# Optimization experiments

Hardware: AMD Instinct MI355X
Metric: run time of the kernel (lower is better)

The kernel has to match this reference:

```python
import jax, jax.numpy as jnp
import numpy as np

NPOINT = 1024   # number of sampled centers
NSAMPLE = 32    # neighbors per center
BN_EPS = 1e-5


def setup_inputs() -> dict:
    key = jax.random.key(0)
    ks = jax.random.split(key, 6)
    B, N, C = 8, 4096, 6
    inp = {
        "xyz": jax.random.normal(ks[0], (B, N, 3), jnp.float32),
        "points": jax.random.normal(ks[1], (B, N, C), jnp.float32),
        "W0": jax.random.normal(ks[2], (64, 9), jnp.float32) * 0.1,
        "g0": jnp.ones((64,), jnp.float32),
        "b0": jnp.zeros((64,), jnp.float32),
        "W1": jax.random.normal(ks[3], (64, 64), jnp.float32) * 0.1,
        "g1": jnp.ones((64,), jnp.float32),
        "b1": jnp.zeros((64,), jnp.float32),
        "W2": jax.random.normal(ks[4], (128, 64), jnp.float32) * 0.1,
        "g2": jnp.ones((128,), jnp.float32),
        "b2": jnp.zeros((128,), jnp.float32),
    }
    return inp


def sample_and_group(xyz, points):
    # xyz: [B,N,3], points: [B,N,C]
    B, N, _ = xyz.shape
    stride = N // NPOINT
    new_xyz = xyz[:, ::stride]                      # [B,S,3] deterministic subsample (FPS surrogate)
    # squared pairwise distances via ||a||^2 + ||b||^2 - 2 a.b  -> [B,S,N]
    d = (jnp.sum(new_xyz * new_xyz, -1)[:, :, None]
         + jnp.sum(xyz * xyz, -1)[:, None, :]
         - 2.0 * jnp.einsum('bsd,bnd->bsn', new_xyz, xyz))
    _, idx = jax.lax.top_k(-d, NSAMPLE)             # [B,S,K] KNN indices
    gather = jax.vmap(lambda arr, i: arr[i])        # per-batch gather: [N,C],[S,K] -> [S,K,C]
    g_xyz = gather(xyz, idx) - new_xyz[:, :, None, :]   # relative coords [B,S,K,3]
    g_pts = gather(points, idx)                     # [B,S,K,C]
    new_points = jnp.concatenate([g_xyz, g_pts], -1)    # [B,S,K,3+C]
    return new_xyz, new_points


def mlp_layer(x, W, g, b):
    # Conv2d(1x1, bias=False) == channel contraction; BN2d with batch stats; ReLU
    x = jnp.einsum('bskc,oc->bsko', x, W)
    m = jnp.mean(x, axis=(0, 1, 2))
    v = jnp.var(x, axis=(0, 1, 2))
    x = (x - m) * jax.lax.rsqrt(v + BN_EPS) * g + b
    return jax.nn.relu(x)


def reference(xyz, points, W0, g0, b0, W1, g1, b1, W2, g2, b2):
    new_xyz, x = sample_and_group(xyz, points)      # x: [B,S,K,9]
    x = mlp_layer(x, W0, g0, b0)
    x = mlp_layer(x, W1, g1, b1)
    x = mlp_layer(x, W2, g2, b2)
    new_points = jnp.max(x, axis=2)                 # max-pool over neighbor dim K -> [B,S,128]
    return new_xyz, new_points
```

## Files before the change

kernel.cpp:

```cpp
#include <hip/hip_runtime.h>
#include <float.h>
#include <stdint.h>

#define TOT   262144
#define NPTS  4096
#define KNN   32
#define BN_EPS 1e-5f
#define CAPV  64
#define TILEP 2048

typedef _Float16 f16;
typedef _Float16 f16x2 __attribute__((ext_vector_type(2)));
typedef _Float16 f16x4 __attribute__((ext_vector_type(4)));
typedef _Float16 f16x8 __attribute__((ext_vector_type(8)));
typedef float    f32x4 __attribute__((ext_vector_type(4)));

__device__ __forceinline__ int mbcnt64(unsigned long long m){
  return __builtin_amdgcn_mbcnt_hi((unsigned)(m>>32),
         __builtin_amdgcn_mbcnt_lo((unsigned)(m & 0xffffffffull), 0));
}
__device__ __forceinline__ unsigned f2ord(float f){
  unsigned u = __float_as_uint(f);
  return u ^ (((unsigned)((int)u >> 31)) | 0x80000000u);
}
__device__ __forceinline__ f16x2 bnrelu2(f16x2 x, f16x2 a, f16x2 c){
  f16x2 r = x*a + c;
  const f16 z = (f16)0.f;
  r[0] = r[0] > z ? r[0] : z;
  r[1] = r[1] > z ? r[1] : z;
  return r;
}
__device__ __forceinline__ void writeElem(int n, int e, float qx, float qy, float qz,
    const float* __restrict__ xb3, const float* __restrict__ fb,
    f16* __restrict__ grouped, f16* __restrict__ g16){
  float px = xb3[n*3+0], py = xb3[n*3+1], pz = xb3[n*3+2];
  f16 a[16];
  a[0]=(f16)(px-qx); a[1]=(f16)(py-qy); a[2]=(f16)(pz-qz);
  #pragma unroll
  for (int c6=0;c6<6;c6++) a[3+c6] = (f16)fb[n*6+c6];
  #pragma unroll
  for (int i=9;i<16;i++) a[i]=(f16)0.f;
  #pragma unroll
  for (int c=0;c<9;c++) grouped[c*TOT+e] = a[c];
  f16x8 lo, hi;
  #pragma unroll
  for (int i=0;i<8;i++){ lo[i]=a[i]; hi[i]=a[8+i]; }
  *(f16x8*)(g16 + (size_t)e*16)     = lo;
  *(f16x8*)(g16 + (size_t)e*16 + 8) = hi;
}

__global__ __launch_bounds__(256) void knn_gather(
    const float* __restrict__ xyz, const float* __restrict__ pts,
    f16* __restrict__ grouped, f16* __restrict__ g16,
    float* __restrict__ out_newxyz){
  __shared__ float4 tile[TILEP];
  __shared__ unsigned wk[8][CAPV];
  __shared__ unsigned short wi[8][CAPV];
  __shared__ unsigned lcnt[8];
  const int tid = threadIdx.x, lane = tid & 63, wv = tid >> 6;
  const int q0 = blockIdx.x*8 + wv*2;
  const int b  = (blockIdx.x*8) >> 10;
  const float* xb3 = xyz + (size_t)b*NPTS*3;
  float qx[2],qy[2],qz[2],qq[2];
  #pragma unroll
  for (int t=0;t<2;t++){
    int n = ((q0+t) & 1023)*4;
    qx[t]=xb3[n*3+0]; qy[t]=xb3[n*3+1]; qz[t]=xb3[n*3+2];
    qq[t]=qx[t]*qx[t]+qy[t]*qy[t]+qz[t]*qz[t];
  }
  if (tid < 8) lcnt[tid] = 0;
  if (lane == 0){
    #pragma unroll
    for (int t=0;t<2;t++){
      out_newxyz[(q0+t)*3+0]=qx[t]; out_newxyz[(q0+t)*3+1]=qy[t];
      out_newxyz[(q0+t)*3+2]=qz[t];
    }
  }

  float dmin[2] = {FLT_MAX, FLT_MAX};
  #pragma unroll 1
  for (int r=0; r<2; ++r){
    __syncthreads();
    #pragma unroll
    for (int k=0;k<8;k++){
      int p = r*TILEP + k*256 + tid;
      float x = xb3[p*3+0], y = xb3[p*3+1], z = xb3[p*3+2];
      tile[k*256+tid] = make_float4(x,y,z, x*x+y*y+z*z);
    }
    __syncthreads();
    #pragma unroll 4
    for (int i=0;i<32;i++){
      float4 P = tile[i*64+lane];
      #pragma unroll
      for (int t=0;t<2;t++){
        float d = (qq[t]+P.w) - 2.f*(qx[t]*P.x+qy[t]*P.y+qz[t]*P.z);
        dmin[t] = d < dmin[t] ? d : dmin[t];
      }
    }
  }
  float sm[2] = {dmin[0], dmin[1]};
  #pragma unroll
  for (int k=2;k<=64;k<<=1){
    #pragma unroll
    for (int j=k>>1;j>0;j>>=1){
      bool keepmin = (((lane&k)==0) == ((lane&j)==0));
      #pragma unroll
      for (int t=0;t<2;t++){
        float o = __shfl_xor(sm[t], j, 64);
        sm[t] = keepmin ? fminf(sm[t],o) : fmaxf(sm[t],o);
      }
    }
  }
  float Uf[2];
  #pragma unroll
  for (int t=0;t<2;t++) Uf[t] = __shfl(sm[t], 31, 64);

  #pragma unroll 1
  for (int r=0; r<2; ++r){
    __syncthreads();
    #pragma unroll
    for (int k=0;k<8;k++){
      int p = r*TILEP + k*256 + tid;
      float x = xb3[p*3+0], y = xb3[p*3+1], z = xb3[p*3+2];
      tile[k*256+tid] = make_float4(x,y,z, x*x+y*y+z*z);
    }
    __syncthreads();
    #pragma unroll 2
    for (int i=0;i<32;i++){
      float4 P = tile[i*64+lane];
      #pragma unroll
      for (int t=0;t<2;t++){
        float d = (qq[t]+P.w) - 2.f*(qx[t]*P.x+qy[t]*P.y+qz[t]*P.z);
        if (d <= Uf[t]){
          unsigned p2 = atomicAdd(&lcnt[wv*2+t], 1u);
          if (p2 < CAPV){
            wk[wv*2+t][p2] = f2ord(d);
            wi[wv*2+t][p2] = (unsigned short)(r*TILEP + i*64 + lane);
          }
        }
      }
    }
  }
  int cnt[2] = {(int)lcnt[wv*2], (int)lcnt[wv*2+1]};

  unsigned long long v[2];
  #pragma unroll
  for (int t=0;t<2;t++){
    unsigned myk = (lane<cnt[t]) ? wk[wv*2+t][lane] : 0xFFFFFFFFu;
    unsigned myi = (lane<cnt[t]) ? wi[wv*2+t][lane] : 0u;
    v[t] = (((unsigned long long)myk)<<16) | myi;
  }
  #pragma unroll
  for (int k=2;k<=64;k<<=1){
    #pragma unroll
    for (int j=k>>1;j>0;j>>=1){
      bool keepmin = (((lane&k)==0) == ((lane&j)==0));
      #pragma unroll
      for (int t=0;t<2;t++){
        unsigned long long o = __shfl_xor(v[t], j, 64);
        v[t] = keepmin ? (v[t]<o?v[t]:o) : (v[t]>o?v[t]:o);
      }
    }
  }

  const float* fb = pts + (size_t)b*NPTS*6;
  #pragma unroll 1
  for (int t=0;t<2;t++){
    const int ebase = (q0+t)*KNN;
    if (cnt[t] <= CAPV){
      if (lane < KNN){
        int n = (int)(v[t] & 0xffffull);
        writeElem(n, ebase+lane, qx[t],qy[t],qz[t], xb3, fb, grouped, g16);
      }
    } else {
      unsigned V=0;
      for (int bit=31; bit>=0; --bit){
        unsigned X = V | (1u<<bit);
        int c=0;
        for (int j=0;j<64;j++){
          int n = j*64+lane;
          float px=xb3[n*3], py=xb3[n*3+1], pz=xb3[n*3+2];
          float d = qq[t] + (px*px+py*py+pz*pz)
                  - 2.f*(qx[t]*px+qy[t]*py+qz[t]*pz);
          c += __popcll(__ballot(f2ord(d) < X));
        }
        if (c < KNN) V = X;
      }
      int cnt2=0;
      for (int pass=0; pass<2; ++pass){
        for (int j=0;j<64;j++){
          int n = j*64+lane;
          float px=xb3[n*3], py=xb3[n*3+1], pz=xb3[n*3+2];
          float d = qq[t] + (px*px+py*py+pz*pz)
                  - 2.f*(qx[t]*px+qy[t]*py+qz[t]*pz);
          unsigned kk = f2ord(d);
          bool sel = pass ? (kk==V) : (kk<V);
          unsigned long long msk = __ballot(sel);
          int pos = cnt2 + mbcnt64(msk);
          if (sel && pos < KNN)
            writeElem(n, ebase+pos, qx[t],qy[t],qz[t], xb3, fb, grouped, g16);
          cnt2 += __popcll(msk);
        }
      }
    }
  }
}

__global__ __launch_bounds__(256) void stats0m(const f16* __restrict__ grouped,
    float* __restrict__ s0m){
  const int lane = threadIdx.x & 63, wv = threadIdx.x >> 6;
  const int c = lane & 15, q = lane >> 4;
  const int base = (blockIdx.x*4 + wv)*512;
  f16x8 cfill = {};
  if (c == 9){
    #pragma unroll
    for (int i=0;i<8;i++) cfill[i] = (f16)1.f;
  }
  f32x4 acc = {0.f,0.f,0.f,0.f};
  #pragma unroll 4
  for (int chunk=0; chunk<16; ++chunk){
    int e = base + chunk*32 + q*8;
    f16x8 f = cfill;
    if (c < 9) f = *(const f16x8*)(grouped + (size_t)c*TOT + e);
    acc = __builtin_amdgcn_mfma_f32_16x16x32_f16(f, f, acc, 0,0,0);
  }
  __shared__ float red[4][16][16];
  #pragma unroll
  for (int i=0;i<4;i++) red[wv][q*4+i][c] = acc[i];
  __syncthreads();
  const int tid = threadIdx.x;
  if (tid < 160){
    int row = tid>>4, col = tid&15;
    float vv = red[0][row][col]+red[1][row][col]+red[2][row][col]+red[3][row][col];
    atomicAdd(&s0m[tid], vv);
  }
}

__global__ void finalize0(const float* __restrict__ s0m,
    const float* __restrict__ W0, const float* __restrict__ g0,
    const float* __restrict__ b0, float* __restrict__ ac0,
    const float* __restrict__ W1, const float* __restrict__ W2,
    f16* __restrict__ W0h, f16* __restrict__ W1h, f16* __restrict__ W2h){
  const int tid = threadIdx.x;
  __shared__ float S[160];
  __shared__ float A0s[64];
  if (tid < 160) S[tid] = s0m[tid];
  __syncthreads();
  if (tid < 64){
    float w[9];
    #pragma unroll
    for (int c=0;c<9;c++) w[c]=W0[tid*9+c];
    const float inv = 1.f/(float)TOT;
    float m=0.f;
    #pragma unroll
    for (int c=0;c<9;c++) m = fmaf(w[c], S[c*16+9], m);
    m *= inv;
    float e2=0.f;
    #pragma unroll
    for (int c1=0;c1<9;c1++){
      float t=0.f;
      #pragma unroll
      for (int c2=0;c2<9;c2++) t = fmaf(w[c2], S[c1*16+c2], t);
      e2 = fmaf(w[c1], t, e2);
    }
    e2 *= inv;
    float var = e2 - m*m;
    float a = g0[tid]*rsqrtf(var + BN_EPS);
    ac0[tid]    = a;
    ac0[64+tid] = fmaf(-m, a, b0[tid]);
    A0s[tid]    = a;
  }
  __syncthreads();
  for (int i=tid; i<2048; i+=256){
    int o = i>>5, c = i&31;
    W0h[i] = (f16)(c<9 ? A0s[o]*W0[o*9+c] : 0.f);
  }
  for (int i=tid; i<4096; i+=256) W1h[i] = (f16)W1[i];
  for (int i=tid; i<8192; i+=256) W2h[i] = (f16)W2[i];
}

__global__ __launch_bounds__(256, 2) void layer1s(
    const f16* __restrict__ g16, const f16* __restrict__ W0h,
    const f16* __restrict__ W1h, const float* __restrict__ ac0,
    float* __restrict__ s1g){
  __shared__ f16 sW0[2048];
  __shared__ f16 sW1[4096];
  __shared__ float ac0c[64];
  __shared__ f16 hb0[4][16][72];
  __shared__ float sred[4][128];
  const int tid = threadIdx.x;
  const int lane = tid & 63, wv = tid >> 6;
  const int e16 = lane & 15, q = lane >> 4;
  *(f16x8*)(&sW0[tid*8]) = *(const f16x8*)(W0h + tid*8);
  *(f16x8*)(&sW1[tid*8])        = *(const f16x8*)(W1h + tid*8);
  *(f16x8*)(&sW1[2048 + tid*8]) = *(const f16x8*)(W1h + 2048 + tid*8);
  if (tid < 64) ac0c[tid] = ac0[64+tid];
  __syncthreads();

  const int base = blockIdx.x*256 + wv*64;
  float ssum[16], ssq[16];
  #pragma unroll
  for (int i=0;i<16;i++){ ssum[i]=0.f; ssq[i]=0.f; }

  #pragma unroll 1
  for (int sub=0; sub<4; ++sub){
    int elem = base + sub*16 + e16;
    f16x8 bg = {};
    if (q < 2) bg = *(const f16x8*)(g16 + (size_t)elem*16 + q*8);
    #pragma unroll
    for (int m=0;m<4;m++){
      f32x4 acc = *(const f32x4*)(&ac0c[m*16 + q*4]);
      f16x8 A0f = *(const f16x8*)(&sW0[(m*16+e16)*32 + q*8]);
      acc = __builtin_amdgcn_mfma_f32_16x16x32_f16(A0f, bg, acc, 0,0,0);
      f16x4 w;
      w[0]=(f16)fmaxf(acc[0],0.f); w[1]=(f16)fmaxf(acc[1],0.f);
      w[2]=(f16)fmaxf(acc[2],0.f); w[3]=(f16)fmaxf(acc[3],0.f);
      *(f16x4*)(&hb0[wv][e16][m*16 + q*4]) = w;
    }
    f32x4 acc2[4];
    #pragma unroll
    for (int m=0;m<4;m++) acc2[m] = (f32x4){0.f,0.f,0.f,0.f};
    #pragma unroll
    for (int s=0;s<2;s++){
      f16x8 bh = *(const f16x8*)(&hb0[wv][e16][s*32 + q*8]);
      #pragma unroll
      for (int m=0;m<4;m++){
        f16x8 A1f = *(const f16x8*)(&sW1[(m*16+e16)*64 + s*32 + q*8]);
        acc2[m] = __builtin_amdgcn_mfma_f32_16x16x32_f16(A1f, bh, acc2[m], 0,0,0);
      }
    }
    #pragma unroll
    for (int m=0;m<4;m++)
      #pragma unroll
      for (int i=0;i<4;i++){
        float x = acc2[m][i];
        ssum[m*4+i] += x;
        ssq[m*4+i]  = fmaf(x, x, ssq[m*4+i]);
      }
  }
  #pragma unroll
  for (int t=0;t<16;t++){
    float a = ssum[t], bq = ssq[t];
    #pragma unroll
    for (int off=1; off<16; off<<=1){
      a  += __shfl_xor(a,  off, 64);
      bq += __shfl_xor(bq, off, 64);
    }
    ssum[t]=a; ssq[t]=bq;
  }
  if (e16==0){
    #pragma unroll
    for (int m=0;m<4;m++)
      #pragma unroll
      for (int i=0;i<4;i++){
        int ch = m*16 + q*4 + i;
        sred[wv][ch]    = ssum[m*4+i];
        sred[wv][64+ch] = ssq[m*4+i];
      }
  }
  __syncthreads();
  if (tid < 128){
    float v = sred[0][tid]+sred[1][tid]+sred[2][tid]+sred[3][tid];
    atomicAdd(&s1g[tid], v);
  }
}

__global__ __launch_bounds__(256, 2) void layer2max(
    const f16* __restrict__ g16, const f16* __restrict__ W0h,
    const f16* __restrict__ W1h, const f16* __restrict__ W2h,
    const float* __restrict__ ac0, const float* __restrict__ s1g,
    const float* __restrict__ g1, const float* __restrict__ b1,
    float* __restrict__ maxbuf, float* __restrict__ s2g){
  __shared__ f16 sW0[2048];
  __shared__ f16 sW1[4096];
  __shared__ float ac0c[64];
  __shared__ f16 ac1s[128];
  __shared__ f16 hb0[4][16][72];
  __shared__ f16 hb1[4][2][16][72];
  float (*redbuf)[256] = (float(*)[256])hb0;
  const int tid = threadIdx.x;
  const int lane = tid & 63, wv = tid >> 6;
  const int e16 = lane & 15, q = lane >> 4;
  *(f16x8*)(&sW0[tid*8]) = *(const f16x8*)(W0h + tid*8);
  *(f16x8*)(&sW1[tid*8])        = *(const f16x8*)(W1h + tid*8);
  *(f16x8*)(&sW1[2048 + tid*8]) = *(const f16x8*)(W1h + 2048 + tid*8);
  if (tid < 64) ac0c[tid] = ac0[64+tid];
  if (tid < 64){
    const float inv = 1.f/(float)TOT;
    float m = s1g[tid]*inv;
    float vv = s1g[64+tid]*inv - m*m;
    float a = g1[tid]*rsqrtf(vv + BN_EPS);
    ac1s[tid]    = (f16)a;
    ac1s[64+tid] = (f16)fmaf(-m, a, b1[tid]);
  }
  __syncthreads();

  f16x8 Bw[8][2];
  #pragma unroll
  for (int nt=0;nt<8;nt++)
    #pragma unroll
    for (int s=0;s<2;s++) Bw[nt][s] = *(const f16x8*)(W2h + (nt*16+e16)*64 + s*32 + q*8);

  float ssum[8], ssq[8];
  #pragma unroll
  for (int i=0;i<8;i++){ ssum[i]=0.f; ssq[i]=0.f; }

  #pragma unroll 1
  for (int qq=0; qq<2; ++qq){
    const int qid = blockIdx.x*8 + wv*2 + qq;
    #pragma unroll 1
    for (int mt=0; mt<2; ++mt){
      int elem = qid*32 + mt*16 + e16;
      f16x8 bg = {};
      if (q < 2) bg = *(const f16x8*)(g16 + (size_t)elem*16 + q*8);
      #pragma unroll
      for (int m=0;m<4;m++){
        f32x4 acc = *(const f32x4*)(&ac0c[m*16 + q*4]);
        f16x8 A0f = *(const f16x8*)(&sW0[(m*16+e16)*32 + q*8]);
        acc = __builtin_amdgcn_mfma_f32_16x16x32_f16(A0f, bg, acc, 0,0,0);
        f16x4 w;
        w[0]=(f16)fmaxf(acc[0],0.f); w[1]=(f16)fmaxf(acc[1],0.f);
        w[2]=(f16)fmaxf(acc[2],0.f); w[3]=(f16)fmaxf(acc[3],0.f);
        *(f16x4*)(&hb0[wv][e16][m*16 + q*4]) = w;
      }
      f32x4 acc2[4];
      #pragma unroll
      for (int m=0;m<4;m++) acc2[m] = (f32x4){0.f,0.f,0.f,0.f};
      #pragma unroll
      for (int s=0;s<2;s++){
        f16x8 bh = *(const f16x8*)(&hb0[wv][e16][s*32 + q*8]);
        #pragma unroll
        for (int m=0;m<4;m++){
          f16x8 A1f = *(const f16x8*)(&sW1[(m*16+e16)*64 + s*32 + q*8]);
          acc2[m] = __builtin_amdgcn_mfma_f32_16x16x32_f16(A1f, bh, acc2[m], 0,0,0);
        }
      }
      #pragma unroll
      for (int m=0;m<4;m++){
        f16x4 a4 = *(const f16x4*)(&ac1s[m*16 + q*4]);
        f16x4 c4 = *(const f16x4*)(&ac1s[64 + m*16 + q*4]);
        f16x2 p0 = bnrelu2((f16x2){(f16)acc2[m][0], (f16)acc2[m][1]},
                           (f16x2){a4[0],a4[1]}, (f16x2){c4[0],c4[1]});
        f16x2 p1 = bnrelu2((f16x2){(f16)acc2[m][2], (f16)acc2[m][3]},
                           (f16x2){a4[2],a4[3]}, (f16x2){c4[2],c4[3]});
        f16x4 w; w[0]=p0[0]; w[1]=p0[1]; w[2]=p1[0]; w[3]=p1[1];
        *(f16x4*)(&hb1[wv][mt][e16][m*16 + q*4]) = w;
      }
    }
    float mx[8];
    #pragma unroll
    for (int g=0; g<2; ++g){
      f32x4 acc3[4][2];
      #pragma unroll
      for (int j=0;j<4;j++){ acc3[j][0]=(f32x4){0,0,0,0}; acc3[j][1]=(f32x4){0,0,0,0}; }
      #pragma unroll
      for (int mt=0; mt<2; ++mt)
        #pragma unroll
        for (int s=0;s<2;s++){
          f16x8 af = *(const f16x8*)(&hb1[wv][mt][e16][s*32 + q*8]);
          #pragma unroll
          for (int j=0;j<4;j++)
            acc3[j][mt] = __builtin_amdgcn_mfma_f32_16x16x32_f16(af, Bw[g*4+j][s], acc3[j][mt], 0,0,0);
        }
      #pragma unroll
      for (int j=0;j<4;j++){
        int nt = g*4 + j;
        f32x4 u = acc3[j][0], vv = acc3[j][1];
        float m1 = fmaxf(fmaxf(u[0],u[1]), fmaxf(u[2],u[3]));
        float m2 = fmaxf(fmaxf(vv[0],vv[1]), fmaxf(vv[2],vv[3]));
        float m = fmaxf(m1, m2);
        ssum[nt] += (u[0]+u[1])+(u[2]+u[3]) + (vv[0]+vv[1])+(vv[2]+vv[3]);
        float sq = 0.f;
        #pragma unroll
        for (int i=0;i<4;i++){ sq = fmaf(u[i],u[i],sq); sq = fmaf(vv[i],vv[i],sq); }
        ssq[nt] += sq;
        m = fmaxf(m, __shfl_xor(m, 16, 64));
        m = fmaxf(m, __shfl_xor(m, 32, 64));
        mx[nt] = m;
      }
    }
    if (lane < 16){
      #pragma unroll
      for (int nt=0;nt<8;nt++) maxbuf[(size_t)qid*128 + nt*16 + lane] = mx[nt];
    }
  }
  #pragma unroll
  for (int nt=0;nt<8;nt++){
    ssum[nt] += __shfl_xor(ssum[nt], 16, 64);
    ssum[nt] += __shfl_xor(ssum[nt], 32, 64);
    ssq[nt]  += __shfl_xor(ssq[nt], 16, 64);
    ssq[nt]  += __shfl_xor(ssq[nt], 32, 64);
  }
  __syncthreads();
  if (q==0){
    #pragma unroll
    for (int nt=0;nt<8;nt++){
      redbuf[wv][nt*16+e16]     = ssum[nt];
      redbuf[wv][128+nt*16+e16] = ssq[nt];
    }
  }
  __syncthreads();
  float v = redbuf[0][tid]+redbuf[1][tid]+redbuf[2][tid]+redbuf[3][tid];
  atomicAdd(&s2g[tid], v);
}

__global__ __launch_bounds__(256) void apply2(
    const float4* __restrict__ maxbuf4, const float* __restrict__ s2g,
    const float* __restrict__ g2, const float* __restrict__ b2,
    float4* __restrict__ outp4){
  __shared__ float a2s[128], c2s[128];
  const int tid = threadIdx.x;
  if (tid < 128){
    const float inv = 1.f/(float)TOT;
    float m = s2g[tid]*inv;
    float v = s2g[128+tid]*inv - m*m;
    float a = g2[tid]*rsqrtf(v + BN_EPS);
    a2s[tid] = a;
    c2s[tid] = fmaf(-m, a, b2[tid]);
  }
  __syncthreads();
  int i = blockIdx.x*256 + tid;
  int c4 = (i & 31)*4;
  float4 m = maxbuf4[i];
  float4 r;
  r.x = fmaxf(fmaf(m.x, a2s[c4+0], c2s[c4+0]), 0.f);
  r.y = fmaxf(fmaf(m.y, a2s[c4+1], c2s[c4+1]), 0.f);
  r.z = fmaxf(fmaf(m.z, a2s[c4+2], c2s[c4+2]), 0.f);
  r.w = fmaxf(fmaf(m.w, a2s[c4+3], c2s[c4+3]), 0.f);
  outp4[i] = r;
}

extern "C" void kernel_launch(void* const* d_in, const int* in_sizes, int n_in,
                              void* d_out, int out_size, void* d_ws, size_t ws_size,
                              hipStream_t stream){
  const float* xyz = (const float*)d_in[0];
  const float* pts = (const float*)d_in[1];
  const float* W0  = (const float*)d_in[2];
  const float* g0  = (const float*)d_in[3];
  const float* b0  = (const float*)d_in[4];
  const float* W1  = (const float*)d_in[5];
  const float* g1  = (const float*)d_in[6];
  const float* b1  = (const float*)d_in[7];
  const float* W2  = (const float*)d_in[8];
  const float* g2  = (const float*)d_in[9];
  const float* b2  = (const float*)d_in[10];
  float* out = (float*)d_out;

  float* ws      = (float*)d_ws;
  f16*   grouped = (f16*)ws;
  f16*   g16     = (f16*)(ws + (size_t)5*TOT);
  float* maxbuf  = ws + (size_t)13*TOT;
  float* basep   = ws + (size_t)17*TOT;
  f16*   W0h     = (f16*)basep;
  f16*   W1h     = (f16*)(basep + 1024);
  f16*   W2h     = (f16*)(basep + 3072);
  float* s0m     = basep + 7168;
  float* s1g     = s0m + 160;
  float* s2g     = s1g + 128;
  float* ac0     = s2g + 256;

  (void)hipMemsetAsync(s0m, 0, 544*sizeof(float), stream);
  knn_gather<<<1024, 256, 0, stream>>>(xyz, pts, grouped, g16, out);
  stats0m   <<< 128, 256, 0, stream>>>(grouped, s0m);
  finalize0 <<<   1, 256, 0, stream>>>(s0m, W0, g0, b0, ac0, W1, W2, W0h, W1h, W2h);
  layer1s   <<<1024, 256, 0, stream>>>(g16, W0h, W1h, ac0, s1g);
  layer2max <<<1024, 256, 0, stream>>>(g16, W0h, W1h, W2h, ac0, s1g, g1, b1, maxbuf, s2g);
  apply2    <<<1024, 256, 0, stream>>>((const float4*)maxbuf, s2g, g2, b2, (float4*)(out + 24576));
}
```

Before: 197.8 us.

## Cache KNN distances in fp16 registers and fold BN0 finalize into layer kernels

The KNN kernel now keeps every candidate distance in an fp16 register array during the first pass. It then filters against a slightly widened threshold from those registers, so the second tile reload and full distance recompute go away. Exact fp32 distances are recomputed only for candidates that pass, reading from global memory. Separately, the single-block finalize0 launch is removed: each layer1s/layer2max block recomputes the BN0 coefficients and fp16 weight conversions itself, trading one serial launch for redundant per-block work. The 128-register array with launch bounds of 4 blocks per unit risks register spills and lower occupancy.

```diff
diff --git a/kernel.cpp b/kernel.cpp
--- a/kernel.cpp
+++ b/kernel.cpp
@@ -49,7 +49,7 @@
   *(f16x8*)(g16 + (size_t)e*16 + 8) = hi;
 }
 
-__global__ __launch_bounds__(256) void knn_gather(
+__global__ __launch_bounds__(256, 4) void knn_gather(
     const float* __restrict__ xyz, const float* __restrict__ pts,
     f16* __restrict__ grouped, f16* __restrict__ g16,
     float* __restrict__ out_newxyz){
@@ -78,7 +78,8 @@
   }
 
   float dmin[2] = {FLT_MAX, FLT_MAX};
-  #pragma unroll 1
+  f16x2 dreg[64];
+  #pragma unroll
   for (int r=0; r<2; ++r){
     __syncthreads();
     #pragma unroll
@@ -88,14 +89,17 @@
       tile[k*256+tid] = make_float4(x,y,z, x*x+y*y+z*z);
     }
     __syncthreads();
-    #pragma unroll 4
+    #pragma unroll
     for (int i=0;i<32;i++){
       float4 P = tile[i*64+lane];
+      f16x2 dh;
       #pragma unroll
       for (int t=0;t<2;t++){
         float d = (qq[t]+P.w) - 2.f*(qx[t]*P.x+qy[t]*P.y+qz[t]*P.z);
         dmin[t] = d < dmin[t] ? d : dmin[t];
-      }
+        dh[t] = (f16)d;
+      }
+      dreg[r*32+i] = dh;
     }
   }
   float sm[2] = {dmin[0], dmin[1]};
@@ -111,33 +115,31 @@
       }
     }
   }
+  f16 uh[2];
   float Uf[2];
   #pragma unroll
-  for (int t=0;t<2;t++) Uf[t] = __shfl(sm[t], 31, 64);
-
-  #pragma unroll 1
-  for (int r=0; r<2; ++r){
-    __syncthreads();
-    #pragma unroll
-    for (int k=0;k<8;k++){
-      int p = r*TILEP + k*256 + tid;
-      float x = xb3[p*3+0], y = xb3[p*3+1], z = xb3[p*3+2];
-      tile[k*256+tid] = make_float4(x,y,z, x*x+y*y+z*z);
-    }
-    __syncthreads();
-    #pragma unroll 2
-    for (int i=0;i<32;i++){
-      float4 P = tile[i*64+lane];
-      #pragma unroll
-      for (int t=0;t<2;t++){
-        float d = (qq[t]+P.w) - 2.f*(qx[t]*P.x+qy[t]*P.y+qz[t]*P.z);
-        if (d <= Uf[t]){
-          unsigned p2 = atomicAdd(&lcnt[wv*2+t], 1u);
-          if (p2 < CAPV){
-            wk[wv*2+t][p2] = f2ord(d);
-            wi[wv*2+t][p2] = (unsigned short)(r*TILEP + i*64 + lane);
-          }
-        }
+  for (int t=0;t<2;t++){
+    Uf[t] = __shfl(sm[t], 31, 64);
+    uh[t] = (f16)(Uf[t] + fmaxf(fabsf(Uf[t])*0.001953125f, 1e-6f));
+  }
+
+  #pragma unroll
+  for (int i=0;i<64;i++){
+    f16x2 dh = dreg[i];
+    bool h0 = dh[0] <= uh[0], h1 = dh[1] <= uh[1];
+    if (h0 || h1){
+      int n = (i>>5)*TILEP + (i&31)*64 + lane;
+      float px = xb3[n*3+0], py = xb3[n*3+1], pz = xb3[n*3+2];
+      float pw = px*px+py*py+pz*pz;
+      if (h0){
+        float d = (qq[0]+pw) - 2.f*(qx[0]*px+qy[0]*py+qz[0]*pz);
+        unsigned p2 = atomicAdd(&lcnt[wv*2+0], 1u);
+        if (p2 < CAPV){ wk[wv*2+0][p2]=f2ord(d); wi[wv*2+0][p2]=(unsigned short)n; }
+      }
+      if (h1){
+        float d = (qq[1]+pw) - 2.f*(qx[1]*px+qy[1]*py+qz[1]*pz);
+        unsigned p2 = atomicAdd(&lcnt[wv*2+1], 1u);
+        if (p2 < CAPV){ wk[wv*2+1][p2]=f2ord(d); wi[wv*2+1][p2]=(unsigned short)n; }
       }
     }
   }
@@ -236,15 +238,11 @@
   }
 }
 
-__global__ void finalize0(const float* __restrict__ s0m,
+__device__ __forceinline__ void bn0_coeffs(int tid, const float* __restrict__ s0m,
     const float* __restrict__ W0, const float* __restrict__ g0,
-    const float* __restrict__ b0, float* __restrict__ ac0,
-    const float* __restrict__ W1, const float* __restrict__ W2,
-    f16* __restrict__ W0h, f16* __restrict__ W1h, f16* __restrict__ W2h){
-  const int tid = threadIdx.x;
-  __shared__ float S[160];
-  __shared__ float A0s[64];
-  if (tid < 160) S[tid] = s0m[tid];
+    const float* __restrict__ b0, float* __restrict__ A0s,
+    float* __restrict__ ac0c, float* __restrict__ Ssh){
+  if (tid < 160) Ssh[tid] = s0m[tid];
   __syncthreads();
   if (tid < 64){
     float w[9];
@@ -253,48 +251,48 @@
     const float inv = 1.f/(float)TOT;
     float m=0.f;
     #pragma unroll
-    for (int c=0;c<9;c++) m = fmaf(w[c], S[c*16+9], m);
+    for (int c=0;c<9;c++) m = fmaf(w[c], Ssh[c*16+9], m);
     m *= inv;
     float e2=0.f;
     #pragma unroll
     for (int c1=0;c1<9;c1++){
       float t=0.f;
       #pragma unroll
-      for (int c2=0;c2<9;c2++) t = fmaf(w[c2], S[c1*16+c2], t);
+      for (int c2=0;c2<9;c2++) t = fmaf(w[c2], Ssh[c1*16+c2], t);
       e2 = fmaf(w[c1], t, e2);
     }
     e2 *= inv;
     float var = e2 - m*m;
     float a = g0[tid]*rsqrtf(var + BN_EPS);
-    ac0[tid]    = a;
-    ac0[64+tid] = fmaf(-m, a, b0[tid]);
-    A0s[tid]    = a;
-  }
-  __syncthreads();
-  for (int i=tid; i<2048; i+=256){
-    int o = i>>5, c = i&31;
-    W0h[i] = (f16)(c<9 ? A0s[o]*W0[o*9+c] : 0.f);
-  }
-  for (int i=tid; i<4096; i+=256) W1h[i] = (f16)W1[i];
-  for (int i=tid; i<8192; i+=256) W2h[i] = (f16)W2[i];
+    A0s[tid]  = a;
+    ac0c[tid] = fmaf(-m, a, b0[tid]);
+  }
+  __syncthreads();
 }
 
 __global__ __launch_bounds__(256, 2) void layer1s(
-    const f16* __restrict__ g16, const f16* __restrict__ W0h,
-    const f16* __restrict__ W1h, const float* __restrict__ ac0,
+    const f16* __restrict__ g16, const float* __restrict__ s0m,
+    const float* __restrict__ W0, const float* __restrict__ g0,
+    const float* __restrict__ b0, const float* __restrict__ W1,
     float* __restrict__ s1g){
   __shared__ f16 sW0[2048];
   __shared__ f16 sW1[4096];
   __shared__ float ac0c[64];
+  __shared__ float A0s[64];
+  __shared__ float Ssh[160];
   __shared__ f16 hb0[4][16][72];
   __shared__ float sred[4][128];
   const int tid = threadIdx.x;
   const int lane = tid & 63, wv = tid >> 6;
   const int e16 = lane & 15, q = lane >> 4;
-  *(f16x8*)(&sW0[tid*8]) = *(const f16x8*)(W0h + tid*8);
-  *(f16x8*)(&sW1[tid*8])        = *(const f16x8*)(W1h + tid*8);
-  *(f16x8*)(&sW1[2048 + tid*8]) = *(const f16x8*)(W1h + 2048 + tid*8);
-  if (tid < 64) ac0c[tid] = ac0[64+tid];
+  bn0_coeffs(tid, s0m, W0, g0, b0, A0s, ac0c, Ssh);
+  #pragma unroll
+  for (int idx=tid; idx<2048; idx+=256){
+    int o = idx>>5, c = idx&31;
+    sW0[idx] = (f16)(c<9 ? A0s[o]*W0[o*9+c] : 0.f);
+  }
+  #pragma unroll
+  for (int idx=tid; idx<4096; idx+=256) sW1[idx] = (f16)W1[idx];
   __syncthreads();
 
   const int base = blockIdx.x*256 + wv*64;
@@ -366,14 +364,17 @@
 }
 
 __global__ __launch_bounds__(256, 2) void layer2max(
-    const f16* __restrict__ g16, const f16* __restrict__ W0h,
-    const f16* __restrict__ W1h, const f16* __restrict__ W2h,
-    const float* __restrict__ ac0, const float* __restrict__ s1g,
+    const f16* __restrict__ g16, const float* __restrict__ s0m,
+    const float* __restrict__ W0, const float* __restrict__ g0,
+    const float* __restrict__ b0, const float* __restrict__ W1,
+    const float* __restrict__ W2, const float* __restrict__ s1g,
     const float* __restrict__ g1, const float* __restrict__ b1,
     float* __restrict__ maxbuf, float* __restrict__ s2g){
   __shared__ f16 sW0[2048];
   __shared__ f16 sW1[4096];
   __shared__ float ac0c[64];
+  __shared__ float A0s[64];
+  __shared__ float Ssh[160];
   __shared__ f16 ac1s[128];
   __shared__ f16 hb0[4][16][72];
   __shared__ f16 hb1[4][2][16][72];
@@ -381,10 +382,14 @@
   const int tid = threadIdx.x;
   const int lane = tid & 63, wv = tid >> 6;
   const int e16 = lane & 15, q = lane >> 4;
-  *(f16x8*)(&sW0[tid*8]) = *(const f16x8*)(W0h + tid*8);
-  *(f16x8*)(&sW1[tid*8])        = *(const f16x8*)(W1h + tid*8);
-  *(f16x8*)(&sW1[2048 + tid*8]) = *(const f16x8*)(W1h + 2048 + tid*8);
-  if (tid < 64) ac0c[tid] = ac0[64+tid];
+  bn0_coeffs(tid, s0m, W0, g0, b0, A0s, ac0c, Ssh);
+  #pragma unroll
+  for (int idx=tid; idx<2048; idx+=256){
+    int o = idx>>5, c = idx&31;
+    sW0[idx] = (f16)(c<9 ? A0s[o]*W0[o*9+c] : 0.f);
+  }
+  #pragma unroll
+  for (int idx=tid; idx<4096; idx+=256) sW1[idx] = (f16)W1[idx];
   if (tid < 64){
     const float inv = 1.f/(float)TOT;
     float m = s1g[tid]*inv;
@@ -399,7 +404,13 @@
   #pragma unroll
   for (int nt=0;nt<8;nt++)
     #pragma unroll
-    for (int s=0;s<2;s++) Bw[nt][s] = *(const f16x8*)(W2h + (nt*16+e16)*64 + s*32 + q*8);
+    for (int s=0;s<2;s++){
+      const float* src = W2 + (nt*16+e16)*64 + s*32 + q*8;
+      f16x8 f;
+      #pragma unroll
+      for (int j=0;j<8;j++) f[j] = (f16)src[j];
+      Bw[nt][s] = f;
+    }
 
   float ssum[8], ssq[8];
   #pragma unroll
@@ -550,20 +561,14 @@
   f16*   grouped = (f16*)ws;
   f16*   g16     = (f16*)(ws + (size_t)5*TOT);
   float* maxbuf  = ws + (size_t)13*TOT;
-  float* basep   = ws + (size_t)17*TOT;
-  f16*   W0h     = (f16*)basep;
-  f16*   W1h     = (f16*)(basep + 1024);
-  f16*   W2h     = (f16*)(basep + 3072);
-  float* s0m     = basep + 7168;
+  float* s0m     = ws + (size_t)17*TOT;
   float* s1g     = s0m + 160;
   float* s2g     = s1g + 128;
-  float* ac0     = s2g + 256;
 
   (void)hipMemsetAsync(s0m, 0, 544*sizeof(float), stream);
   knn_gather<<<1024, 256, 0, stream>>>(xyz, pts, grouped, g16, out);
   stats0m   <<< 128, 256, 0, stream>>>(grouped, s0m);
-  finalize0 <<<   1, 256, 0, stream>>>(s0m, W0, g0, b0, ac0, W1, W2, W0h, W1h, W2h);
-  layer1s   <<<1024, 256, 0, stream>>>(g16, W0h, W1h, ac0, s1g);
-  layer2max <<<1024, 256, 0, stream>>>(g16, W0h, W1h, W2h, ac0, s1g, g1, b1, maxbuf, s2g);
+  layer1s   <<<1024, 256, 0, stream>>>(g16, s0m, W0, g0, b0, W1, s1g);
+  layer2max <<<1024, 256, 0, stream>>>(g16, s0m, W0, g0, b0, W1, W2, s1g, g1, b1, maxbuf, s2g);
   apply2    <<<1024, 256, 0, stream>>>((const float4*)maxbuf, s2g, g2, b2, (float4*)(out + 24576));
 }
```

Result: slower. 261.2 us (+32.1%).
